# Optimization experiments

Measured on AMD Instinct MI355X. Metric: run time of the kernel, lower is better.

## Reference

```python
import jax, jax.numpy as jnp
import numpy as np

CLASS_NUM = 512
B = 1024
E = 50000


def setup_inputs() -> dict:
    key = jax.random.key(0)
    k1, k2, k3, k4 = jax.random.split(key, 4)
    hr = jax.random.normal(k1, (B, CLASS_NUM), dtype=jnp.float32)
    tail = jax.random.normal(k2, (E, CLASS_NUM), dtype=jnp.float32)
    # Linear(2*class_num, 1): weight [1, 2*class_num], bias [1]
    bound = 1.0 / np.sqrt(2 * CLASS_NUM)
    W = jax.random.uniform(k3, (1, 2 * CLASS_NUM), dtype=jnp.float32, minval=-bound, maxval=bound)
    b = jax.random.uniform(k4, (1,), dtype=jnp.float32, minval=-bound, maxval=bound)
    return {"hr_class_embedding": hr, "tail_class_embedding": tail, "W": W, "b": b}


def reference(hr_class_embedding, tail_class_embedding, W, b):
    # scores[i, j] = Linear(concat(hr_i, tail_j)) = hr_i @ W1 + tail_j @ W2 + b
    C = hr_class_embedding.shape[1]
    W1 = W[0, :C]   # [C]
    W2 = W[0, C:]   # [C]
    hr_part = hr_class_embedding @ W1      # [B]
    tail_part = tail_class_embedding @ W2  # [E]
    scores = hr_part[:, None] + tail_part[None, :] + b[0]  # [B, E]
    return (scores, 0)
```

## Files before the change

kernel.cpp:

```cpp
#include <hip/hip_runtime.h>

#define BN 1024
#define EN 50000
#define CN 512

typedef float v4f __attribute__((ext_vector_type(4)));

__global__ __launch_bounds__(256) void dots_kernel(
    const float* __restrict__ hr,
    const float* __restrict__ tail,
    const float* __restrict__ W,
    const float* __restrict__ bptr,
    float* __restrict__ parts,
    float* __restrict__ out)
{
    const int gtid = blockIdx.x * blockDim.x + threadIdx.x;
    const int wave = gtid >> 6;
    const int lane = threadIdx.x & 63;
    if (wave >= EN + BN) return;

    const v4f* r4;
    const v4f* w4;
    if (wave < EN) {
        r4 = (const v4f*)(tail + (size_t)wave * CN);
        w4 = (const v4f*)(W + CN);
    } else {
        r4 = (const v4f*)(hr + (size_t)(wave - EN) * CN);
        w4 = (const v4f*)W;
    }

    v4f a0 = r4[lane];
    v4f a1 = r4[lane + 64];
    v4f b0 = w4[lane];
    v4f b1 = w4[lane + 64];

    v4f p = a0 * b0 + a1 * b1;
    float sum = p.x + p.y + p.z + p.w;

    #pragma unroll
    for (int off = 32; off > 0; off >>= 1)
        sum += __shfl_down(sum, off, 64);

    if (lane == 0) {
        if (wave < EN) parts[wave] = sum;
        else           parts[wave] = sum + bptr[0];
    }
    if (gtid == 0) out[(size_t)BN * EN] = 0.0f;
}

__global__ __launch_bounds__(512) void bcast_kernel(
    const float* __restrict__ parts,
    float* __restrict__ out)
{
    const int i = blockIdx.x;
    const float hv = parts[EN + i];
    const v4f* t4 = (const v4f*)parts;
    v4f* orow = (v4f*)(out + (size_t)i * EN);

    int j4 = threadIdx.x;
    #pragma unroll 4
    for (int it = 0; it < 24; ++it, j4 += 512) {
        orow[j4] = t4[j4] + hv;
    }
    if (j4 < EN / 4) {
        orow[j4] = t4[j4] + hv;
    }
}

extern "C" void kernel_launch(void* const* d_in, const int* in_sizes, int n_in,
                              void* d_out, int out_size, void* d_ws, size_t ws_size,
                              hipStream_t stream)
{
    const float* hr   = (const float*)d_in[0];
    const float* tail = (const float*)d_in[1];
    const float* W    = (const float*)d_in[2];
    const float* b    = (const float*)d_in[3];
    float* out = (float*)d_out;
    float* parts = (float*)d_ws;

    const int total_waves = EN + BN;
    const int blocks1 = (total_waves + 3) / 4;
    dots_kernel<<<blocks1, 256, 0, stream>>>(hr, tail, W, b, parts, out);

    bcast_kernel<<<BN, 512, 0, stream>>>(parts, out);
}
```

Before: 291.5 us.

## Fuse tail dot products with output broadcast in column-tiled kernel

```diff
diff --git a/kernel.cpp b/kernel.cpp
--- a/kernel.cpp
+++ b/kernel.cpp
@@ -3,67 +3,78 @@
 #define BN 1024
 #define EN 50000
 #define CN 512
+#define JT 64
 
 typedef float v4f __attribute__((ext_vector_type(4)));
 
-__global__ __launch_bounds__(256) void dots_kernel(
+__global__ __launch_bounds__(256) void hr_kernel(
     const float* __restrict__ hr,
-    const float* __restrict__ tail,
     const float* __restrict__ W,
     const float* __restrict__ bptr,
-    float* __restrict__ parts,
+    float* __restrict__ hr_parts,
     float* __restrict__ out)
 {
     const int gtid = blockIdx.x * blockDim.x + threadIdx.x;
     const int wave = gtid >> 6;
     const int lane = threadIdx.x & 63;
-    if (wave >= EN + BN) return;
 
-    const v4f* r4;
-    const v4f* w4;
-    if (wave < EN) {
-        r4 = (const v4f*)(tail + (size_t)wave * CN);
-        w4 = (const v4f*)(W + CN);
-    } else {
-        r4 = (const v4f*)(hr + (size_t)(wave - EN) * CN);
-        w4 = (const v4f*)W;
-    }
+    const v4f* r4 = (const v4f*)(hr + (size_t)wave * CN);
+    const v4f* w4 = (const v4f*)W;
 
-    v4f a0 = r4[lane];
-    v4f a1 = r4[lane + 64];
-    v4f b0 = w4[lane];
-    v4f b1 = w4[lane + 64];
-
-    v4f p = a0 * b0 + a1 * b1;
+    v4f p = r4[lane] * w4[lane] + r4[lane + 64] * w4[lane + 64];
     float sum = p.x + p.y + p.z + p.w;
 
     #pragma unroll
     for (int off = 32; off > 0; off >>= 1)
         sum += __shfl_down(sum, off, 64);
 
-    if (lane == 0) {
-        if (wave < EN) parts[wave] = sum;
-        else           parts[wave] = sum + bptr[0];
-    }
+    if (lane == 0) hr_parts[wave] = sum + bptr[0];
     if (gtid == 0) out[(size_t)BN * EN] = 0.0f;
 }
 
-__global__ __launch_bounds__(512) void bcast_kernel(
-    const float* __restrict__ parts,
+__global__ __launch_bounds__(256) void fused_kernel(
+    const float* __restrict__ tail,
+    const float* __restrict__ W,
+    const float* __restrict__ hr_parts,
     float* __restrict__ out)
 {
-    const int i = blockIdx.x;
-    const float hv = parts[EN + i];
-    const v4f* t4 = (const v4f*)parts;
-    v4f* orow = (v4f*)(out + (size_t)i * EN);
+    __shared__ float tails[JT];
 
-    int j4 = threadIdx.x;
+    const int j0   = blockIdx.x * JT;
+    const int w    = threadIdx.x >> 6;
+    const int lane = threadIdx.x & 63;
+
+    const v4f* w4 = (const v4f*)(W + CN);
+    const v4f wb0 = w4[lane];
+    const v4f wb1 = w4[lane + 64];
+
     #pragma unroll 4
-    for (int it = 0; it < 24; ++it, j4 += 512) {
-        orow[j4] = t4[j4] + hv;
+    for (int r = 0; r < 16; ++r) {
+        const int j = j0 + w * 16 + r;
+        if (j < EN) {
+            const v4f* r4 = (const v4f*)(tail + (size_t)j * CN);
+            v4f p = r4[lane] * wb0 + r4[lane + 64] * wb1;
+            float sum = p.x + p.y + p.z + p.w;
+            #pragma unroll
+            for (int off = 32; off > 0; off >>= 1)
+                sum += __shfl_down(sum, off, 64);
+            if (lane == 0) tails[w * 16 + r] = sum;
+        }
     }
-    if (j4 < EN / 4) {
-        orow[j4] = t4[j4] + hv;
+    __syncthreads();
+
+    const int g = threadIdx.x >> 4;
+    const int c = threadIdx.x & 15;
+    const int j = j0 + c * 4;
+    if (j < EN) {
+        const v4f tj = *(const v4f*)&tails[c * 4];
+        float* obase = out + (size_t)g * 64 * EN + j;
+        #pragma unroll 4
+        for (int p = 0; p < 64; ++p) {
+            const float hv = hr_parts[g * 64 + p];
+            v4f o = tj + hv;
+            *(v4f*)(obase + (size_t)p * EN) = o;
+        }
     }
 }
 
@@ -76,11 +87,10 @@
     const float* W    = (const float*)d_in[2];
     const float* b    = (const float*)d_in[3];
     float* out = (float*)d_out;
-    float* parts = (float*)d_ws;
+    float* hr_parts = (float*)d_ws;
 
-    const int total_waves = EN + BN;
-    const int blocks1 = (total_waves + 3) / 4;
-    dots_kernel<<<blocks1, 256, 0, stream>>>(hr, tail, W, b, parts, out);
+    hr_kernel<<<256, 256, 0, stream>>>(hr, W, b, hr_parts, out);
 
-    bcast_kernel<<<BN, 512, 0, stream>>>(parts, out);
+    const int blocks = (EN + JT - 1) / JT;
+    fused_kernel<<<blocks, 256, 0, stream>>>(tail, W, hr_parts, out);
 }
```

New measurement: 307.0 us. 5.3% more time.
